# Kernel optimization log

Hardware: AMD Instinct MI355X
Metric: run time of the kernel (lower is better)

## Reference

```python
import jax, jax.numpy as jnp
import numpy as np

D_MODEL = 1024
N_HEADS = 16
D_FF = 4096
LN_EPS = 1e-5


def _linear_params(key, d_in, d_out):
    kw, kb = jax.random.split(key)
    bound = 1.0 / np.sqrt(d_in)
    W = jax.random.uniform(kw, (d_out, d_in), jnp.float32, -bound, bound)
    b = jax.random.uniform(kb, (d_out,), jnp.float32, -bound, bound)
    return W, b


def setup_inputs() -> dict:
    key = jax.random.key(0)
    ks = jax.random.split(key, 8)
    x = jax.random.normal(ks[0], (2, 2048, D_MODEL), jnp.float32)
    Wq, bq = _linear_params(ks[1], D_MODEL, D_MODEL)
    Wk, bk = _linear_params(ks[2], D_MODEL, D_MODEL)
    Wv, bv = _linear_params(ks[3], D_MODEL, D_MODEL)
    Wo, bo = _linear_params(ks[4], D_MODEL, D_MODEL)
    W1, b1 = _linear_params(ks[5], D_MODEL, D_FF)
    W2, b2 = _linear_params(ks[6], D_FF, D_MODEL)
    ln1_g = jnp.ones((D_MODEL,), jnp.float32)
    ln1_b = jnp.zeros((D_MODEL,), jnp.float32)
    ln2_g = jnp.ones((D_MODEL,), jnp.float32)
    ln2_b = jnp.zeros((D_MODEL,), jnp.float32)
    return dict(x=x, Wq=Wq, bq=bq, Wk=Wk, bk=bk, Wv=Wv, bv=bv, Wo=Wo, bo=bo,
                ln1_g=ln1_g, ln1_b=ln1_b, W1=W1, b1=b1, W2=W2, b2=b2,
                ln2_g=ln2_g, ln2_b=ln2_b)


def _layernorm(x, g, b):
    mu = jnp.mean(x, axis=-1, keepdims=True)
    var = jnp.mean(jnp.square(x - mu), axis=-1, keepdims=True)
    return (x - mu) * jax.lax.rsqrt(var + LN_EPS) * g + b


def _lin(x, W, b):
    return jnp.einsum('bsd,ed->bse', x, W) + b


def _attn(x, Wq, bq, Wk, bk, Wv, bv, Wo, bo):
    B, S, _ = x.shape
    d_head = D_MODEL // N_HEADS
    scale = d_head ** -0.5
    split = lambda t: t.reshape(B, S, N_HEADS, d_head).transpose(0, 2, 1, 3)
    q = split(_lin(x, Wq, bq))  # b h s d
    k = split(_lin(x, Wk, bk))
    v = split(_lin(x, Wv, bv))
    scores = jnp.einsum('bhqd,bhkd->bhqk', q, k) * scale
    attn = jax.nn.softmax(scores, axis=-1)
    out = jnp.einsum('bhqk,bhkd->bhqd', attn, v)
    out = out.transpose(0, 2, 1, 3).reshape(B, S, D_MODEL)
    return _lin(out, Wo, bo)


def reference(x, Wq, bq, Wk, bk, Wv, bv, Wo, bo, ln1_g, ln1_b, W1, b1, W2, b2, ln2_g, ln2_b):
    x = x + _attn(_layernorm(x, ln1_g, ln1_b), Wq, bq, Wk, bk, Wv, bv, Wo, bo)
    h = _layernorm(x, ln2_g, ln2_b)
    h = _lin(h, W1, b1)
    h = jax.nn.gelu(h, approximate=False)
    h = _lin(h, W2, b2)
    return x + h
```

## Files before the change

### kernel.cpp

```cpp
#include <hip/hip_runtime.h>
#include <hip/hip_bf16.h>
#include <stdint.h>

#define DM 1024
#define DFF 4096
#define NH 16
#define DH 64
#define SEQ 2048
#define MROWS 4096

typedef unsigned short u16;
typedef __attribute__((ext_vector_type(8))) short bf16x8;
typedef __attribute__((ext_vector_type(4))) float f32x4;
typedef __attribute__((ext_vector_type(4))) unsigned short u16x4;

__device__ __forceinline__ u16 f2b(float f) {
  union { float f; uint32_t u; } v; v.f = f;
  uint32_t r = v.u + 0x7FFFu + ((v.u >> 16) & 1u);
  return (u16)(r >> 16);
}

__device__ __forceinline__ u16 f2bn(float f) {
  __hip_bfloat16 h = __float2bfloat16(f);
  return *reinterpret_cast<u16*>(&h);
}

__device__ __forceinline__ void gl_lds16(const void* g, void* l) {
  __builtin_amdgcn_global_load_lds(
      (const __attribute__((address_space(1))) uint32_t*)g,
      (__attribute__((address_space(3))) uint32_t*)l, 16, 0, 0);
}

struct CvtArgs { const float* src[6]; u16* dst[6]; int n4[6]; };

__global__ void cvt_kernel(CvtArgs a) {
  const int stride = gridDim.x * blockDim.x;
  const int t0 = blockIdx.x * blockDim.x + threadIdx.x;
  for (int i = 0; i < 6; ++i) {
    const float4* s = (const float4*)a.src[i];
    u16x4* d = (u16x4*)a.dst[i];
    const int n = a.n4[i];
    for (int idx = t0; idx < n; idx += stride) {
      float4 v = s[idx];
      u16x4 o;
      o[0] = f2b(v.x); o[1] = f2b(v.y); o[2] = f2b(v.z); o[3] = f2b(v.w);
      d[idx] = o;
    }
  }
}

__global__ __launch_bounds__(256)
void ln_kernel(const float* __restrict__ x, const float* __restrict__ g,
               const float* __restrict__ be, u16* __restrict__ out) {
  const int row = blockIdx.x;
  const int tid = threadIdx.x;
  const float4 v = ((const float4*)(x + (size_t)row * DM))[tid];
  float s  = v.x + v.y + v.z + v.w;
  float s2 = v.x * v.x + v.y * v.y + v.z * v.z + v.w * v.w;
  #pragma unroll
  for (int m = 1; m < 64; m <<= 1) {
    s  += __shfl_xor(s,  m, 64);
    s2 += __shfl_xor(s2, m, 64);
  }
  __shared__ float red[8];
  const int w = tid >> 6, lane = tid & 63;
  if (lane == 0) { red[w] = s; red[4 + w] = s2; }
  __syncthreads();
  s  = red[0] + red[1] + red[2] + red[3];
  s2 = red[4] + red[5] + red[6] + red[7];
  const float mu  = s * (1.0f / DM);
  const float var = s2 * (1.0f / DM) - mu * mu;
  const float rstd = rsqrtf(var + 1e-5f);
  const float4 gv = ((const float4*)g)[tid];
  const float4 bv = ((const float4*)be)[tid];
  u16x4 o;
  o[0] = f2b((v.x - mu) * rstd * gv.x + bv.x);
  o[1] = f2b((v.y - mu) * rstd * gv.y + bv.y);
  o[2] = f2b((v.z - mu) * rstd * gv.z + bv.z);
  o[3] = f2b((v.w - mu) * rstd * gv.w + bv.w);
  ((u16x4*)(out + (size_t)row * DM))[tid] = o;
}

__global__ __launch_bounds__(256)
void combine_kernel(const float4* __restrict__ p0, const float4* __restrict__ p1,
                    const float4* __restrict__ bias, const float4* __restrict__ resid,
                    float4* __restrict__ out, int total4, int colmask4) {
  for (int i = blockIdx.x * 256 + threadIdx.x; i < total4; i += gridDim.x * 256) {
    float4 a = p0[i], b = p1[i], bs = bias[i & colmask4], rr = resid[i];
    float4 o;
    o.x = a.x + b.x + bs.x + rr.x;
    o.y = a.y + b.y + bs.y + rr.y;
    o.z = a.z + b.z + bs.z + rr.z;
    o.w = a.w + b.w + bs.w + rr.w;
    out[i] = o;
  }
}

__global__ __launch_bounds__(256)
void combine_ln_kernel(const float4* __restrict__ p0, const float4* __restrict__ p1,
                       const float4* __restrict__ bias, const float4* __restrict__ resid,
                       float4* __restrict__ xout,
                       const float* __restrict__ g, const float* __restrict__ be,
                       u16* __restrict__ nout) {
  const int row = blockIdx.x;
  const int tid = threadIdx.x;
  const int i = row * (DM / 4) + tid;
  const float4 a = p0[i], b = p1[i], bs = bias[tid], rr = resid[i];
  float4 v;
  v.x = a.x + b.x + bs.x + rr.x;
  v.y = a.y + b.y + bs.y + rr.y;
  v.z = a.z + b.z + bs.z + rr.z;
  v.w = a.w + b.w + bs.w + rr.w;
  xout[i] = v;
  float s  = v.x + v.y + v.z + v.w;
  float s2 = v.x * v.x + v.y * v.y + v.z * v.z + v.w * v.w;
  #pragma unroll
  for (int m = 1; m < 64; m <<= 1) {
    s  += __shfl_xor(s,  m, 64);
    s2 += __shfl_xor(s2, m, 64);
  }
  __shared__ float red[8];
  const int w = tid >> 6, lane = tid & 63;
  if (lane == 0) { red[w] = s; red[4 + w] = s2; }
  __syncthreads();
  s  = red[0] + red[1] + red[2] + red[3];
  s2 = red[4] + red[5] + red[6] + red[7];
  const float mu  = s * (1.0f / DM);
  const float var = s2 * (1.0f / DM) - mu * mu;
  const float rstd = rsqrtf(var + 1e-5f);
  const float4 gv = ((const float4*)g)[tid];
  const float4 bv = ((const float4*)be)[tid];
  u16x4 o;
  o[0] = f2b((v.x - mu) * rstd * gv.x + bv.x);
  o[1] = f2b((v.y - mu) * rstd * gv.y + bv.y);
  o[2] = f2b((v.z - mu) * rstd * gv.z + bv.z);
  o[3] = f2b((v.w - mu) * rstd * gv.w + bv.w);
  ((u16x4*)(nout + (size_t)row * DM))[tid] = o;
}

struct GemmPtrs { const u16* W[3]; const float* bias[3]; void* out[3];
                  const float* resid; int vtrans; };

template<int EPI>
__global__ __launch_bounds__(256)
void gemm_bt(const u16* __restrict__ A, GemmPtrs p, int M, int N,
             int Kstride, int Kchunk) {
  __shared__ __align__(16) u16 As[128 * 64];
  __shared__ __align__(16) u16 Bs[128 * 64];
  const u16* __restrict__ Wm = p.W[blockIdx.z];
  const float* __restrict__ bias = p.bias[blockIdx.z];
  void* outv = p.out[blockIdx.z];
  const float* resid = p.resid;

  const int tid = threadIdx.x;
  const int lane = tid & 63;
  const int w = tid >> 6;
  const int brow = blockIdx.y * 128;
  const int bcol = blockIdx.x * 128;
  const int wr = (w >> 1) * 64, wc = (w & 1) * 64;
  const int koff = (EPI == 3) ? blockIdx.z * Kchunk : 0;

  f32x4 acc[4][4] = {};

  const int srow = lane >> 3;
  const int scol = (lane & 7) * 8;
  const int nkt = Kchunk >> 6;
  for (int kt = 0; kt < nkt; ++kt) {
    const int k0 = koff + kt * 64;
    #pragma unroll
    for (int i = 0; i < 4; ++i) {
      const int r = i * 32 + w * 8;
      gl_lds16(&A [(size_t)(brow + r + srow) * Kstride + k0 + scol], &As[r * 64]);
      gl_lds16(&Wm[(size_t)(bcol + r + srow) * Kstride + k0 + scol], &Bs[r * 64]);
    }
    __syncthreads();
    #pragma unroll
    for (int ks = 0; ks < 2; ++ks) {
      const int ko = ks * 32 + (lane >> 4) * 8;
      bf16x8 a[4], b[4];
      #pragma unroll
      for (int f = 0; f < 4; ++f)
        a[f] = *(const bf16x8*)&As[(wr + f * 16 + (lane & 15)) * 64 + ko];
      #pragma unroll
      for (int f = 0; f < 4; ++f)
        b[f] = *(const bf16x8*)&Bs[(wc + f * 16 + (lane & 15)) * 64 + ko];
      #pragma unroll
      for (int fr = 0; fr < 4; ++fr)
        #pragma unroll
        for (int fc = 0; fc < 4; ++fc)
          acc[fr][fc] = __builtin_amdgcn_mfma_f32_16x16x32_bf16(a[fr], b[fc], acc[fr][fc], 0, 0, 0);
    }
    __syncthreads();
  }

  const int orow0 = brow + wr + (lane >> 4) * 4;
  const int ocol0 = bcol + wc + (lane & 15);

  if (EPI == 0 && p.vtrans && blockIdx.z == 2) {
    #pragma unroll
    for (int fr = 0; fr < 4; ++fr) {
      const int row0 = orow0 + fr * 16;
      const int bq = row0 >> 11, s0 = row0 & (SEQ - 1);
      #pragma unroll
      for (int fc = 0; fc < 4; ++fc) {
        const int col = ocol0 + fc * 16;
        const float bvv = bias[col];
        u16x4 o;
        #pragma unroll
        for (int r = 0; r < 4; ++r) o[r] = f2b(acc[fr][fc][r] + bvv);
        *(u16x4*)((u16*)outv + (size_t)(bq * DM + col) * SEQ + s0) = o;
      }
    }
    return;
  }

  const float oscale = (EPI == 0 && p.vtrans && blockIdx.z == 0) ? 0.125f : 1.0f;

  #pragma unroll
  for (int fr = 0; fr < 4; ++fr) {
    #pragma unroll
    for (int fc = 0; fc < 4; ++fc) {
      const int col = ocol0 + fc * 16;
      const float bvv = (EPI == 3) ? 0.0f : bias[col];
      #pragma unroll
      for (int r = 0; r < 4; ++r) {
        const int row = orow0 + fr * 16 + r;
        const size_t idx = (size_t)row * N + col;
        float v = acc[fr][fc][r] + bvv;
        if (EPI == 0) {
          ((u16*)outv)[idx] = f2b(v * oscale);
        } else if (EPI == 1) {
          float ge = 0.5f * v * (1.0f + erff(v * 0.70710678118654752f));
          ((u16*)outv)[idx] = f2b(ge);
        } else if (EPI == 2) {
          ((float*)outv)[idx] = v + resid[idx];
        } else {
          ((float*)outv)[idx] = v;
        }
      }
    }
  }
}

__global__ __launch_bounds__(256, 4)
void attn_kernel(const u16* __restrict__ Q, const u16* __restrict__ K,
                 const u16* __restrict__ Vt, u16* __restrict__ O) {
  __shared__ __align__(16) u16 Ks[64 * 64];
  __shared__ __align__(16) u16 Vts[64 * 64];
  __shared__ __align__(16) u16 Ps[4][16 * 64];
  const int tid = threadIdx.x, lane = tid & 63, w = tid >> 6;
  const int bh = blockIdx.y, b = bh >> 4, h = bh & 15;
  const int q0 = blockIdx.x * 64 + w * 16;
  const size_t base = (size_t)b * SEQ * DM + (size_t)h * DH;
  const size_t vbase = (size_t)(b * DM + h * DH) * SEQ;

  const int l15 = lane & 15, hi = lane >> 4, l7 = lane & 7;
  const int kf[2] = { (hi ^ l7) * 8, ((4 + hi) ^ l7) * 8 };

  bf16x8 qf[2];
  {
    const size_t qrow = base + (size_t)(q0 + l15) * DM;
    #pragma unroll
    for (int ks = 0; ks < 2; ++ks)
      qf[ks] = *(const bf16x8*)&Q[qrow + ks * 32 + hi * 8];
  }

  f32x4 oacc[4] = {};
  float mrow[4], lpart[4];
  #pragma unroll
  for (int r = 0; r < 4; ++r) { mrow[r] = -1e30f; lpart[r] = 0.0f; }

  const int srow = lane >> 3;
  const int scol_sw = ((lane & 7) ^ srow) * 8;

  for (int kt = 0; kt < SEQ / 64; ++kt) {
    #pragma unroll
    for (int i = 0; i < 2; ++i) {
      const int r = i * 32 + w * 8;
      gl_lds16(&K[base + (size_t)(kt * 64 + r + srow) * DM + scol_sw], &Ks[r * 64]);
      gl_lds16(&Vt[vbase + (size_t)(r + srow) * SEQ + kt * 64 + scol_sw], &Vts[r * 64]);
    }
    __syncthreads();

    f32x4 sacc[4] = {};
    __builtin_amdgcn_s_setprio(1);
    #pragma unroll
    for (int ks = 0; ks < 2; ++ks) {
      #pragma unroll
      for (int fn = 0; fn < 4; ++fn) {
        bf16x8 kb = *(const bf16x8*)&Ks[(fn * 16 + l15) * 64 + kf[ks]];
        sacc[fn] = __builtin_amdgcn_mfma_f32_16x16x32_bf16(qf[ks], kb, sacc[fn], 0, 0, 0);
      }
    }
    __builtin_amdgcn_s_setprio(0);

    #pragma unroll
    for (int r = 0; r < 4; ++r) {
      float tm = fmaxf(fmaxf(sacc[0][r], sacc[1][r]), fmaxf(sacc[2][r], sacc[3][r]));
      #pragma unroll
      for (int m = 1; m <= 8; m <<= 1) tm = fmaxf(tm, __shfl_xor(tm, m, 64));
      if (__any(tm > mrow[r] + 8.0f)) {
        const float mnew = fmaxf(mrow[r], tm);
        const float fs = __expf(mrow[r] - mnew);
        mrow[r] = mnew;
        lpart[r] *= fs;
        #pragma unroll
        for (int fd = 0; fd < 4; ++fd) oacc[fd][r] *= fs;
      }
      float ps = 0.0f;
      #pragma unroll
      for (int fn = 0; fn < 4; ++fn) {
        float pp = __expf(sacc[fn][r] - mrow[r]);
        sacc[fn][r] = pp;
        ps += pp;
      }
      lpart[r] += ps;
    }

    {
      const int pr = hi * 4;
      #pragma unroll
      for (int fn = 0; fn < 4; ++fn)
        #pragma unroll
        for (int r = 0; r < 4; ++r) {
          const int q = pr + r;
          Ps[w][q * 64 + ((fn * 16 + l15) ^ ((q & 7) << 3))] = f2bn(sacc[fn][r]);
        }
    }
    __builtin_amdgcn_s_setprio(1);
    #pragma unroll
    for (int ks = 0; ks < 2; ++ks) {
      bf16x8 pa = *(const bf16x8*)&Ps[w][l15 * 64 + kf[ks]];
      #pragma unroll
      for (int fd = 0; fd < 4; ++fd) {
        bf16x8 vbf = *(const bf16x8*)&Vts[(fd * 16 + l15) * 64 + kf[ks]];
        oacc[fd] = __builtin_amdgcn_mfma_f32_16x16x32_bf16(pa, vbf, oacc[fd], 0, 0, 0);
      }
    }
    __builtin_amdgcn_s_setprio(0);
    __syncthreads();
  }

  #pragma unroll
  for (int r = 0; r < 4; ++r) {
    #pragma unroll
    for (int m = 1; m <= 8; m <<= 1) lpart[r] += __shfl_xor(lpart[r], m, 64);
  }

  #pragma unroll
  for (int fd = 0; fd < 4; ++fd)
    #pragma unroll
    for (int r = 0; r < 4; ++r) {
      const int row = q0 + hi * 4 + r;
      const float v = oacc[fd][r] / lpart[r];
      O[base + (size_t)row * DM + fd * 16 + l15] = f2bn(v);
    }
}

extern "C" void kernel_launch(void* const* d_in, const int* in_sizes, int n_in,
                              void* d_out, int out_size, void* d_ws, size_t ws_size,
                              hipStream_t stream) {
  const float* x    = (const float*)d_in[0];
  const float* Wq   = (const float*)d_in[1];
  const float* bq   = (const float*)d_in[2];
  const float* Wk   = (const float*)d_in[3];
  const float* bk   = (const float*)d_in[4];
  const float* Wv   = (const float*)d_in[5];
  const float* bv   = (const float*)d_in[6];
  const float* Wo   = (const float*)d_in[7];
  const float* bo   = (const float*)d_in[8];
  const float* ln1g = (const float*)d_in[9];
  const float* ln1b = (const float*)d_in[10];
  const float* W1   = (const float*)d_in[11];
  const float* b1   = (const float*)d_in[12];
  const float* W2   = (const float*)d_in[13];
  const float* b2   = (const float*)d_in[14];
  const float* ln2g = (const float*)d_in[15];
  const float* ln2b = (const float*)d_in[16];
  float* out = (float*)d_out;

  char* wsb = (char*)d_ws;
  size_t off = 0;
  auto alloc = [&](size_t bytes) -> char* {
    char* pp = wsb + off;
    off += (bytes + 255) & ~(size_t)255;
    return pp;
  };
  u16* Wq_b = (u16*)alloc((size_t)DM * DM * 2);
  u16* Wk_b = (u16*)alloc((size_t)DM * DM * 2);
  u16* Wv_b = (u16*)alloc((size_t)DM * DM * 2);
  u16* Wo_b = (u16*)alloc((size_t)DM * DM * 2);
  u16* W1_b = (u16*)alloc((size_t)DFF * DM * 2);
  u16* W2_b = (u16*)alloc((size_t)DM * DFF * 2);
  u16* xn   = (u16*)alloc((size_t)MROWS * DM * 2);
  u16* qb   = (u16*)alloc((size_t)MROWS * DM * 2);
  u16* kb   = (u16*)alloc((size_t)MROWS * DM * 2);
  u16* vt   = (u16*)alloc((size_t)MROWS * DM * 2);
  u16* ao   = (u16*)alloc((size_t)MROWS * DM * 2);
  u16* h1   = (u16*)alloc((size_t)MROWS * DFF * 2);

  float* pA = (float*)xn;
  float* pB = (float*)kb;

  CvtArgs ca;
  ca.src[0] = Wq; ca.dst[0] = Wq_b; ca.n4[0] = DM * DM / 4;
  ca.src[1] = Wk; ca.dst[1] = Wk_b; ca.n4[1] = DM * DM / 4;
  ca.src[2] = Wv; ca.dst[2] = Wv_b; ca.n4[2] = DM * DM / 4;
  ca.src[3] = Wo; ca.dst[3] = Wo_b; ca.n4[3] = DM * DM / 4;
  ca.src[4] = W1; ca.dst[4] = W1_b; ca.n4[4] = DFF * DM / 4;
  ca.src[5] = W2; ca.dst[5] = W2_b; ca.n4[5] = DM * DFF / 4;
  cvt_kernel<<<2048, 256, 0, stream>>>(ca);

  ln_kernel<<<MROWS, 256, 0, stream>>>(x, ln1g, ln1b, xn);

  GemmPtrs pq = {};
  pq.W[0] = Wq_b; pq.W[1] = Wk_b; pq.W[2] = Wv_b;
  pq.bias[0] = bq; pq.bias[1] = bk; pq.bias[2] = bv;
  pq.out[0] = qb; pq.out[1] = kb; pq.out[2] = vt;
  pq.vtrans = 1;
  gemm_bt<0><<<dim3(DM / 128, MROWS / 128, 3), 256, 0, stream>>>(xn, pq, MROWS, DM, DM, DM);

  attn_kernel<<<dim3(SEQ / 64, 2 * NH), 256, 0, stream>>>(qb, kb, vt, ao);

  GemmPtrs po = {};
  po.W[0] = Wo_b; po.W[1] = Wo_b;
  po.bias[0] = bo; po.bias[1] = bo;
  po.out[0] = pA; po.out[1] = pB;
  gemm_bt<3><<<dim3(DM / 128, MROWS / 128, 2), 256, 0, stream>>>(ao, po, MROWS, DM, DM, DM / 2);
  combine_ln_kernel<<<MROWS, 256, 0, stream>>>((const float4*)pA, (const float4*)pB,
                                               (const float4*)bo, (const float4*)x,
                                               (float4*)out, ln2g, ln2b, ao);

  GemmPtrs p1 = {};
  p1.W[0] = W1_b; p1.bias[0] = b1; p1.out[0] = h1;
  gemm_bt<1><<<dim3(DFF / 128, MROWS / 128, 1), 256, 0, stream>>>(ao, p1, MROWS, DFF, DM, DM);

  GemmPtrs p2 = {};
  p2.W[0] = W2_b; p2.W[1] = W2_b;
  p2.bias[0] = b2; p2.bias[1] = b2;
  p2.out[0] = pA; p2.out[1] = pB;
  gemm_bt<3><<<dim3(DM / 128, MROWS / 128, 2), 256, 0, stream>>>(h1, p2, MROWS, DM, DFF, DFF / 2);
  combine_kernel<<<2048, 256, 0, stream>>>((const float4*)pA, (const float4*)pB,
                                           (const float4*)b2, (const float4*)out,
                                           (float4*)out, MROWS * DM / 4, DM / 4 - 1);
}
```

Before: 317.2 us.

## Rewrite attention with 32x32 MFMA, transposed S, and register-resident P

Rewrites the flash-attention kernel so each wave handles 32 query rows using 32x32x16 bf16 MFMAs, with the S tile computed transposed (K as the A operand) so the softmax row max needs only one cross-lane shuffle. P is packed to bf16 and redistributed across lanes with xor-32 shuffles instead of going through LDS, which removes the per-tile P store and reload. Blocks shrink to 2 waves (128 threads) and each covers the same 64 queries. This trades LDS traffic and shuffle reductions for more registers per wave and fewer waves per block, which may lower occupancy and latency hiding.

After: 317.1 us. Within noise of the previous version (-0.0%).

```diff
diff --git a/kernel.cpp b/kernel.cpp
--- a/kernel.cpp
+++ b/kernel.cpp
@@ -12,6 +12,7 @@
 typedef unsigned short u16;
 typedef __attribute__((ext_vector_type(8))) short bf16x8;
 typedef __attribute__((ext_vector_type(4))) float f32x4;
+typedef __attribute__((ext_vector_type(16))) float f32x16;
 typedef __attribute__((ext_vector_type(4))) unsigned short u16x4;
 
 __device__ __forceinline__ u16 f2b(float f) {
@@ -23,6 +24,10 @@
 __device__ __forceinline__ u16 f2bn(float f) {
   __hip_bfloat16 h = __float2bfloat16(f);
   return *reinterpret_cast<u16*>(&h);
+}
+
+__device__ __forceinline__ uint32_t pk2(float lo, float hi) {
+  return (uint32_t)f2bn(lo) | ((uint32_t)f2bn(hi) << 16);
 }
 
 __device__ __forceinline__ void gl_lds16(const void* g, void* l) {
@@ -242,119 +247,124 @@
   }
 }
 
-__global__ __launch_bounds__(256, 4)
+__global__ __launch_bounds__(128, 4)
 void attn_kernel(const u16* __restrict__ Q, const u16* __restrict__ K,
                  const u16* __restrict__ Vt, u16* __restrict__ O) {
   __shared__ __align__(16) u16 Ks[64 * 64];
   __shared__ __align__(16) u16 Vts[64 * 64];
-  __shared__ __align__(16) u16 Ps[4][16 * 64];
   const int tid = threadIdx.x, lane = tid & 63, w = tid >> 6;
   const int bh = blockIdx.y, b = bh >> 4, h = bh & 15;
-  const int q0 = blockIdx.x * 64 + w * 16;
+  const int q0 = blockIdx.x * 64 + w * 32;
   const size_t base = (size_t)b * SEQ * DM + (size_t)h * DH;
   const size_t vbase = (size_t)(b * DM + h * DH) * SEQ;
 
-  const int l15 = lane & 15, hi = lane >> 4, l7 = lane & 7;
-  const int kf[2] = { (hi ^ l7) * 8, ((4 + hi) ^ l7) * 8 };
-
-  bf16x8 qf[2];
+  const int l31 = lane & 31, hi = lane >> 5, l7 = l31 & 7;
+
+  bf16x8 qf[4];
   {
-    const size_t qrow = base + (size_t)(q0 + l15) * DM;
-    #pragma unroll
-    for (int ks = 0; ks < 2; ++ks)
-      qf[ks] = *(const bf16x8*)&Q[qrow + ks * 32 + hi * 8];
-  }
-
-  f32x4 oacc[4] = {};
-  float mrow[4], lpart[4];
+    const size_t qrow = base + (size_t)(q0 + l31) * DM;
+    #pragma unroll
+    for (int dt = 0; dt < 4; ++dt)
+      qf[dt] = *(const bf16x8*)&Q[qrow + dt * 16 + hi * 8];
+  }
+
+  f32x16 oacc[2] = {};
+  float mq = -1e30f, lq = 0.0f;
+
+  for (int kt = 0; kt < SEQ / 64; ++kt) {
+    #pragma unroll
+    for (int i = 0; i < 4; ++i) {
+      const int r0 = w * 32 + i * 8;
+      const int row = r0 + (lane >> 3);
+      const int ch = ((lane & 7) ^ (row & 7)) * 8;
+      gl_lds16(&K[base + (size_t)(kt * 64 + row) * DM + ch], &Ks[r0 * 64]);
+      gl_lds16(&Vt[vbase + (size_t)row * SEQ + kt * 64 + ch], &Vts[r0 * 64]);
+    }
+    __syncthreads();
+
+    #pragma unroll
+    for (int sub = 0; sub < 2; ++sub) {
+      f32x16 sacc = {};
+      __builtin_amdgcn_s_setprio(1);
+      #pragma unroll
+      for (int dt = 0; dt < 4; ++dt) {
+        bf16x8 kf = *(const bf16x8*)&Ks[(sub * 32 + l31) * 64 + (((dt << 1) | hi) ^ l7) * 8];
+        sacc = __builtin_amdgcn_mfma_f32_32x32x16_bf16(kf, qf[dt], sacc, 0, 0, 0);
+      }
+      __builtin_amdgcn_s_setprio(0);
+
+      float tm = sacc[0];
+      #pragma unroll
+      for (int r = 1; r < 16; ++r) tm = fmaxf(tm, sacc[r]);
+      tm = fmaxf(tm, __shfl_xor(tm, 32, 64));
+
+      if (__any(tm > mq + 8.0f)) {
+        const float mnew = fmaxf(mq, tm);
+        const float fs = __expf(mq - mnew);
+        mq = mnew;
+        lq *= fs;
+        #pragma unroll
+        for (int r = 0; r < 16; ++r) {
+          const float fsr = __shfl(fs, (r & 3) + 8 * (r >> 2) + 4 * hi, 64);
+          oacc[0][r] *= fsr;
+          oacc[1][r] *= fsr;
+        }
+      }
+
+      uint32_t wd[2][4];
+      float ps = 0.0f;
+      #pragma unroll
+      for (int half = 0; half < 2; ++half) {
+        float p[8];
+        #pragma unroll
+        for (int j = 0; j < 8; ++j) {
+          p[j] = __expf(sacc[half * 8 + j] - mq);
+          ps += p[j];
+        }
+        const uint32_t a = pk2(p[0], p[1]), c = pk2(p[2], p[3]);
+        const uint32_t bb = pk2(p[4], p[5]), d = pk2(p[6], p[7]);
+        const uint32_t xa = (uint32_t)__shfl_xor((int)a, 32, 64);
+        const uint32_t xb = (uint32_t)__shfl_xor((int)bb, 32, 64);
+        const uint32_t xc = (uint32_t)__shfl_xor((int)c, 32, 64);
+        const uint32_t xd = (uint32_t)__shfl_xor((int)d, 32, 64);
+        wd[half][0] = hi ? xb : a;
+        wd[half][1] = hi ? xd : c;
+        wd[half][2] = hi ? bb : xa;
+        wd[half][3] = hi ? d : xc;
+      }
+      lq += ps;
+      bf16x8 pa0, pa1;
+      #pragma unroll
+      for (int j = 0; j < 4; ++j) {
+        ((uint32_t*)&pa0)[j] = wd[0][j];
+        ((uint32_t*)&pa1)[j] = wd[1][j];
+      }
+
+      __builtin_amdgcn_s_setprio(1);
+      #pragma unroll
+      for (int dt = 0; dt < 2; ++dt) {
+        #pragma unroll
+        for (int ks = 0; ks < 2; ++ks) {
+          bf16x8 vf = *(const bf16x8*)&Vts[(dt * 32 + l31) * 64 +
+                                           (((sub << 2) | (ks << 1) | hi) ^ l7) * 8];
+          oacc[dt] = __builtin_amdgcn_mfma_f32_32x32x16_bf16(ks ? pa1 : pa0, vf, oacc[dt], 0, 0, 0);
+        }
+      }
+      __builtin_amdgcn_s_setprio(0);
+    }
+    __syncthreads();
+  }
+
+  const float ltot = lq + __shfl_xor(lq, 32, 64);
   #pragma unroll
-  for (int r = 0; r < 4; ++r) { mrow[r] = -1e30f; lpart[r] = 0.0f; }
-
-  const int srow = lane >> 3;
-  const int scol_sw = ((lane & 7) ^ srow) * 8;
-
-  for (int kt = 0; kt < SEQ / 64; ++kt) {
-    #pragma unroll
-    for (int i = 0; i < 2; ++i) {
-      const int r = i * 32 + w * 8;
-      gl_lds16(&K[base + (size_t)(kt * 64 + r + srow) * DM + scol_sw], &Ks[r * 64]);
-      gl_lds16(&Vt[vbase + (size_t)(r + srow) * SEQ + kt * 64 + scol_sw], &Vts[r * 64]);
-    }
-    __syncthreads();
-
-    f32x4 sacc[4] = {};
-    __builtin_amdgcn_s_setprio(1);
-    #pragma unroll
-    for (int ks = 0; ks < 2; ++ks) {
-      #pragma unroll
-      for (int fn = 0; fn < 4; ++fn) {
-        bf16x8 kb = *(const bf16x8*)&Ks[(fn * 16 + l15) * 64 + kf[ks]];
-        sacc[fn] = __builtin_amdgcn_mfma_f32_16x16x32_bf16(qf[ks], kb, sacc[fn], 0, 0, 0);
-      }
-    }
-    __builtin_amdgcn_s_setprio(0);
-
-    #pragma unroll
-    for (int r = 0; r < 4; ++r) {
-      float tm = fmaxf(fmaxf(sacc[0][r], sacc[1][r]), fmaxf(sacc[2][r], sacc[3][r]));
-      #pragma unroll
-      for (int m = 1; m <= 8; m <<= 1) tm = fmaxf(tm, __shfl_xor(tm, m, 64));
-      if (__any(tm > mrow[r] + 8.0f)) {
-        const float mnew = fmaxf(mrow[r], tm);
-        const float fs = __expf(mrow[r] - mnew);
-        mrow[r] = mnew;
-        lpart[r] *= fs;
-        #pragma unroll
-        for (int fd = 0; fd < 4; ++fd) oacc[fd][r] *= fs;
-      }
-      float ps = 0.0f;
-      #pragma unroll
-      for (int fn = 0; fn < 4; ++fn) {
-        float pp = __expf(sacc[fn][r] - mrow[r]);
-        sacc[fn][r] = pp;
-        ps += pp;
-      }
-      lpart[r] += ps;
-    }
-
-    {
-      const int pr = hi * 4;
-      #pragma unroll
-      for (int fn = 0; fn < 4; ++fn)
-        #pragma unroll
-        for (int r = 0; r < 4; ++r) {
-          const int q = pr + r;
-          Ps[w][q * 64 + ((fn * 16 + l15) ^ ((q & 7) << 3))] = f2bn(sacc[fn][r]);
-        }
-    }
-    __builtin_amdgcn_s_setprio(1);
-    #pragma unroll
-    for (int ks = 0; ks < 2; ++ks) {
-      bf16x8 pa = *(const bf16x8*)&Ps[w][l15 * 64 + kf[ks]];
-      #pragma unroll
-      for (int fd = 0; fd < 4; ++fd) {
-        bf16x8 vbf = *(const bf16x8*)&Vts[(fd * 16 + l15) * 64 + kf[ks]];
-        oacc[fd] = __builtin_amdgcn_mfma_f32_16x16x32_bf16(pa, vbf, oacc[fd], 0, 0, 0);
-      }
-    }
-    __builtin_amdgcn_s_setprio(0);
-    __syncthreads();
-  }
-
-  #pragma unroll
-  for (int r = 0; r < 4; ++r) {
-    #pragma unroll
-    for (int m = 1; m <= 8; m <<= 1) lpart[r] += __shfl_xor(lpart[r], m, 64);
-  }
-
-  #pragma unroll
-  for (int fd = 0; fd < 4; ++fd)
-    #pragma unroll
-    for (int r = 0; r < 4; ++r) {
-      const int row = q0 + hi * 4 + r;
-      const float v = oacc[fd][r] / lpart[r];
-      O[base + (size_t)row * DM + fd * 16 + l15] = f2bn(v);
-    }
+  for (int r = 0; r < 16; ++r) {
+    const int crow = (r & 3) + 8 * (r >> 2) + 4 * hi;
+    const float lr = __shfl(ltot, crow, 64);
+    const float inv = 1.0f / lr;
+    const size_t orow = base + (size_t)(q0 + crow) * DM;
+    O[orow + l31]      = f2bn(oacc[0][r] * inv);
+    O[orow + 32 + l31] = f2bn(oacc[1][r] * inv);
+  }
 }
 
 extern "C" void kernel_launch(void* const* d_in, const int* in_sizes, int n_in,
@@ -420,7 +430,7 @@
   pq.vtrans = 1;
   gemm_bt<0><<<dim3(DM / 128, MROWS / 128, 3), 256, 0, stream>>>(xn, pq, MROWS, DM, DM, DM);
 
-  attn_kernel<<<dim3(SEQ / 64, 2 * NH), 256, 0, stream>>>(qb, kb, vt, ao);
+  attn_kernel<<<dim3(SEQ / 64, 2 * NH), 128, 0, stream>>>(qb, kb, vt, ao);
 
   GemmPtrs po = {};
   po.W[0] = Wo_b; po.W[1] = Wo_b;
```
